# Kernel optimization log

Measured on AMD Instinct MI355X. Metric: run time of the kernel, lower is better.

Reference implementation:

```python
import jax, jax.numpy as jnp
import numpy as np

N, E, DIN, DOUT = 40000, 640000, 128, 256
BN_EPS = 1e-5  # torch BatchNorm1d default eps


def setup_inputs() -> dict:
    key = jax.random.key(0)
    ks = jax.random.split(key, 16)
    x = jax.random.normal(ks[0], (N, DIN), jnp.float32)
    edge_index = jax.random.randint(ks[1], (2, E), 0, N, dtype=jnp.int32)
    s1 = 1.0 / np.sqrt(DIN)
    s2 = 1.0 / np.sqrt(DOUT)
    return {
        "x": x,
        "edge_index": edge_index,
        "eps": jnp.zeros((), jnp.float32),  # GINConv train_eps init = 0
        "W1": jax.random.normal(ks[2], (DIN, DOUT), jnp.float32) * s1,
        "b1": jnp.zeros((DOUT,), jnp.float32),
        "g1": jnp.ones((DOUT,), jnp.float32),
        "bt1": jnp.zeros((DOUT,), jnp.float32),
        "m1": jax.random.normal(ks[3], (DOUT,), jnp.float32) * 0.1,
        "v1": jax.random.uniform(ks[4], (DOUT,), jnp.float32, 0.5, 1.5),
        "W2": jax.random.normal(ks[5], (DOUT, DOUT), jnp.float32) * s2,
        "b2": jnp.zeros((DOUT,), jnp.float32),
        "g2": jnp.ones((DOUT,), jnp.float32),
        "bt2": jnp.zeros((DOUT,), jnp.float32),
        "m2": jax.random.normal(ks[6], (DOUT,), jnp.float32) * 0.1,
        "v2": jax.random.uniform(ks[7], (DOUT,), jnp.float32, 0.5, 1.5),
        "Wres": jax.random.normal(ks[8], (DIN, DOUT), jnp.float32) * s1,
    }


def _bn(h, g, b, m, v):
    # inference-mode BatchNorm1d with running stats
    return (h - m) * jax.lax.rsqrt(v + BN_EPS) * g + b


def reference(x, edge_index, eps, W1, b1, g1, bt1, m1, v1,
              W2, b2, g2, bt2, m2, v2, Wres):
    src, dst = edge_index[0], edge_index[1]
    # GIN sum aggregation: messages x[src] scatter-added at dst
    agg = jax.ops.segment_sum(x[src], dst, num_segments=N)  # [N, DIN]
    h = (1.0 + eps) * x + agg
    h = jax.nn.relu(_bn(h @ W1 + b1, g1, bt1, m1, v1))       # [N, DOUT]
    h = jax.nn.relu(_bn(h @ W2 + b2, g2, bt2, m2, v2))       # [N, DOUT]
    # dropout is identity in eval mode; residual projection since DIN != DOUT
    return jax.nn.relu(h + x @ Wres)
```

## Files before the change

kernel.cpp:

```cpp
#include <hip/hip_runtime.h>

#define NN 40000
#define NPAD 40064
#define EE 640000
#define KDIN 128
#define KDOUT 256

#define NB 157
#define CAP 6144
#define CAPH 4096

typedef __attribute__((ext_vector_type(8))) short bf16x8;
typedef __attribute__((ext_vector_type(4))) float f32x4;

static __device__ __forceinline__ unsigned short f2bf(float f) {
    union { float f; unsigned int u; } v; v.f = f;
    unsigned int r = (v.u + 0x7FFFu + ((v.u >> 16) & 1u)) >> 16;
    return (unsigned short)r;
}
static __device__ __forceinline__ float bf2f(unsigned short h) {
    union { unsigned int u; float f; } v; v.u = ((unsigned int)h) << 16;
    return v.f;
}

#define PREP_GRID 3021
__global__ __launch_bounds__(256) void k_prep(
    const float* __restrict__ x,
    const float* __restrict__ W1, const float* __restrict__ W2,
    const float* __restrict__ Wres,
    ushort* __restrict__ xb, ushort* __restrict__ wt_all,
    int* __restrict__ cur, ushort* __restrict__ hb) {
    int b = blockIdx.x, tid = threadIdx.x;
    if (b < 2504) {
        int i = b * 256 + tid;
        int row = i >> 4;
        uint4 o = {0, 0, 0, 0};
        if (row < NN) {
            const float4* xp = (const float4*)x + (size_t)i * 2;
            float4 a = xp[0], c = xp[1];
            o.x = (unsigned)f2bf(a.x) | ((unsigned)f2bf(a.y) << 16);
            o.y = (unsigned)f2bf(a.z) | ((unsigned)f2bf(a.w) << 16);
            o.z = (unsigned)f2bf(c.x) | ((unsigned)f2bf(c.y) << 16);
            o.w = (unsigned)f2bf(c.z) | ((unsigned)f2bf(c.w) << 16);
        }
        if (row < NPAD) *(uint4*)(xb + (size_t)i * 8) = o;
    } else if (b < 3016) {
        int j = (b - 2504) * 256 + tid;
        if (j < 32768) {
            int c = j >> 7, r = j & 127;
            wt_all[j] = f2bf(W1[r * KDOUT + c]);
        } else if (j < 98304) {
            int j2 = j - 32768;
            int c = j2 >> 8, r = j2 & 255;
            wt_all[j] = f2bf(W2[r * KDOUT + c]);
        } else {
            int j3 = j - 98304;
            int c = j3 >> 7, r = j3 & 127;
            wt_all[j] = f2bf(Wres[r * KDOUT + c]);
        }
    } else if (b < 3020) {
        int idx = (b - 3016) * 256 + tid;
        ((uint4*)(hb + (size_t)NN * KDIN))[idx] = (uint4){0, 0, 0, 0};
    } else {
        if (tid < NB) cur[tid] = 0;
    }
}

__global__ __launch_bounds__(256) void k_binA(const int* __restrict__ ei,
                                              int* __restrict__ cur,
                                              unsigned int* __restrict__ recs) {
    __shared__ int cnt[160], lstart[160], lcur[160], gbase[160];
    __shared__ int sw[256];
    __shared__ unsigned int lrec[4096];
    __shared__ int laddr[4096];
    int tid = threadIdx.x;
    int e0 = blockIdx.x * 4096;
    int e1 = min(e0 + 4096, EE);
    int ns = e1 - e0;

    if (tid < NB) cnt[tid] = 0;
    __syncthreads();
    for (int s = tid; s < ns; s += 256)
        atomicAdd(&cnt[ei[EE + e0 + s] >> 8], 1);
    __syncthreads();
    sw[tid] = (tid < NB) ? cnt[tid] : 0;
    __syncthreads();
    for (int off = 1; off < 256; off <<= 1) {
        int add = (tid >= off) ? sw[tid - off] : 0;
        __syncthreads();
        sw[tid] += add;
        __syncthreads();
    }
    if (tid < NB) {
        int st = sw[tid] - cnt[tid];
        lstart[tid] = st;
        lcur[tid] = st;
        gbase[tid] = atomicAdd(&cur[tid], cnt[tid]);
    }
    __syncthreads();
    for (int s = tid; s < ns; s += 256) {
        int e = e0 + s;
        int src = ei[e];
        int dst = ei[EE + e];
        int b = dst >> 8;
        int p = atomicAdd(&lcur[b], 1);
        lrec[p] = ((unsigned int)(dst & 255) << 16) | (unsigned int)src;
        laddr[p] = b * CAP + gbase[b] + (p - lstart[b]);
    }
    __syncthreads();
    for (int s = tid; s < ns; s += 256)
        recs[laddr[s]] = lrec[s];
}

__global__ __launch_bounds__(256) void k_aggB(const unsigned int* __restrict__ recs,
                                              const int* __restrict__ cur,
                                              const ushort* __restrict__ xb,
                                              const float* __restrict__ eps,
                                              ushort* __restrict__ hb) {
    __shared__ ushort lsrc[CAPH];
    __shared__ int lcnt[128], lst[128], lcur[128];
    __shared__ int sw[256];
    int tid = threadIdx.x;
    int bi = blockIdx.x;
    int b = bi >> 3, nh = (bi >> 2) & 1, q = bi & 3;
    int cnt = cur[b];
    const unsigned int* rb = recs + (size_t)b * CAP;

    if (tid < 128) lcnt[tid] = 0;
    __syncthreads();
    for (int s = tid; s < cnt; s += 256) {
        int d = rb[s] >> 16;
        if ((d >> 7) == nh) atomicAdd(&lcnt[d & 127], 1);
    }
    __syncthreads();
    sw[tid] = (tid < 128) ? lcnt[tid] : 0;
    __syncthreads();
    for (int off = 1; off < 128; off <<= 1) {
        int add = (tid >= off) ? sw[tid - off] : 0;
        __syncthreads();
        sw[tid] += add;
        __syncthreads();
    }
    if (tid < 128) {
        int e = sw[tid] - lcnt[tid];
        lst[tid] = e;
        lcur[tid] = e;
    }
    __syncthreads();
    for (int s = tid; s < cnt; s += 256) {
        unsigned int r = rb[s];
        int d = r >> 16;
        if ((d >> 7) == nh) {
            int p = atomicAdd(&lcur[d & 127], 1);
            lsrc[p] = (ushort)(r & 0xffff);
        }
    }
    __syncthreads();

    int g = tid >> 2, lane = tid & 3;
    float s1 = 1.0f + eps[0];
    for (int d = g; d < 128; d += 64) {
        int node = b * 256 + nh * 128 + d;
        if (node >= NN) continue;
        int st = lst[d], en = st + lcnt[d];
        uint4 me = *((const uint4*)(xb + (size_t)node * KDIN) + q * 4 + lane);
        float a[8], a2[8];
        a[0] = bf2f((ushort)(me.x & 0xffff)) * s1; a[1] = bf2f((ushort)(me.x >> 16)) * s1;
        a[2] = bf2f((ushort)(me.y & 0xffff)) * s1; a[3] = bf2f((ushort)(me.y >> 16)) * s1;
        a[4] = bf2f((ushort)(me.z & 0xffff)) * s1; a[5] = bf2f((ushort)(me.z >> 16)) * s1;
        a[6] = bf2f((ushort)(me.w & 0xffff)) * s1; a[7] = bf2f((ushort)(me.w >> 16)) * s1;
#pragma unroll
        for (int i = 0; i < 8; ++i) a2[i] = 0.f;
        int e = st;
        for (; e + 1 < en; e += 2) {
            int s0 = lsrc[e], sB = lsrc[e + 1];
            uint4 v0 = *((const uint4*)(xb + (size_t)s0 * KDIN) + q * 4 + lane);
            uint4 v1 = *((const uint4*)(xb + (size_t)sB * KDIN) + q * 4 + lane);
            a[0] += bf2f((ushort)(v0.x & 0xffff)); a[1] += bf2f((ushort)(v0.x >> 16));
            a[2] += bf2f((ushort)(v0.y & 0xffff)); a[3] += bf2f((ushort)(v0.y >> 16));
            a[4] += bf2f((ushort)(v0.z & 0xffff)); a[5] += bf2f((ushort)(v0.z >> 16));
            a[6] += bf2f((ushort)(v0.w & 0xffff)); a[7] += bf2f((ushort)(v0.w >> 16));
            a2[0] += bf2f((ushort)(v1.x & 0xffff)); a2[1] += bf2f((ushort)(v1.x >> 16));
            a2[2] += bf2f((ushort)(v1.y & 0xffff)); a2[3] += bf2f((ushort)(v1.y >> 16));
            a2[4] += bf2f((ushort)(v1.z & 0xffff)); a2[5] += bf2f((ushort)(v1.z >> 16));
            a2[6] += bf2f((ushort)(v1.w & 0xffff)); a2[7] += bf2f((ushort)(v1.w >> 16));
        }
        if (e < en) {
            int s0 = lsrc[e];
            uint4 v0 = *((const uint4*)(xb + (size_t)s0 * KDIN) + q * 4 + lane);
            a[0] += bf2f((ushort)(v0.x & 0xffff)); a[1] += bf2f((ushort)(v0.x >> 16));
            a[2] += bf2f((ushort)(v0.y & 0xffff)); a[3] += bf2f((ushort)(v0.y >> 16));
            a[4] += bf2f((ushort)(v0.z & 0xffff)); a[5] += bf2f((ushort)(v0.z >> 16));
            a[6] += bf2f((ushort)(v0.w & 0xffff)); a[7] += bf2f((ushort)(v0.w >> 16));
        }
#pragma unroll
        for (int i = 0; i < 8; ++i) a[i] += a2[i];
        uint4 o;
        o.x = (unsigned)f2bf(a[0]) | ((unsigned)f2bf(a[1]) << 16);
        o.y = (unsigned)f2bf(a[2]) | ((unsigned)f2bf(a[3]) << 16);
        o.z = (unsigned)f2bf(a[4]) | ((unsigned)f2bf(a[5]) << 16);
        o.w = (unsigned)f2bf(a[6]) | ((unsigned)f2bf(a[7]) << 16);
        *((uint4*)(hb + (size_t)node * KDIN) + q * 4 + lane) = o;
    }
}


#define STAGE_WT(Wt_, Kc_, K2_)                                                 \
    for (int id = tid; id < BNT * (K2_) / 16; id += 256) {                      \
        int c = id / ((K2_) / 16);                                              \
        int koff = (id % ((K2_) / 16)) * 16;                                    \
        uint4 v = *(const uint4*)((const char*)((Wt_) + (size_t)(ncol0 + c) * (Kc_)) + koff); \
        *(uint4*)((char*)s + c * (K2_) + (koff ^ ((c & 7) << 4))) = v;          \
    }

#define MM_LOOP(A_, Kc_, K2_, acc0_, acc1_)                                     \
    {                                                                           \
        const char* a0p = (const char*)((A_) + (size_t)r0 * (Kc_)) + lq * 16;   \
        const char* a1p = a0p + 16 * (Kc_) * 2;                                 \
        for (int k0 = 0; k0 < (Kc_); k0 += 32) {                                \
            bf16x8 a0 = *(const bf16x8*)(a0p + k0 * 2);                         \
            bf16x8 a1 = *(const bf16x8*)(a1p + k0 * 2);                         \
            int kb = (k0 + lq * 8) * 2;                                         \
            _Pragma("unroll")                                                   \
            for (int nt = 0; nt < 8; ++nt) {                                    \
                int c = nt * 16 + l15;                                          \
                bf16x8 b = *(const bf16x8*)((const char*)s + c * (K2_) + (kb ^ ((c & 7) << 4))); \
                acc0_[nt] = __builtin_amdgcn_mfma_f32_16x16x32_bf16(a0, b, acc0_[nt], 0, 0, 0); \
                acc1_[nt] = __builtin_amdgcn_mfma_f32_16x16x32_bf16(a1, b, acc1_[nt], 0, 0, 0); \
            }                                                                   \
        }                                                                       \
    }

#define BNT 128

__global__ __launch_bounds__(256) void k_mm1(
    const ushort* __restrict__ A, const ushort* __restrict__ Wt,
    const float* __restrict__ bb, const float* __restrict__ g,
    const float* __restrict__ bt, const float* __restrict__ m,
    const float* __restrict__ vv, ushort* __restrict__ C) {
    __shared__ ushort s[BNT * 128];
    int tid = threadIdx.x;
    int bm = blockIdx.x >> 1, bn = blockIdx.x & 1;
    int ncol0 = bn * BNT;
    STAGE_WT(Wt, 128, 256);
    __syncthreads();
    int wid = tid >> 6, lane = tid & 63;
    int l15 = lane & 15, lq = lane >> 4;
    int r0 = bm * 128 + wid * 32 + l15;
    f32x4 acc0[8] = {}, acc1[8] = {};
    MM_LOOP(A, 128, 256, acc0, acc1);
#pragma unroll
    for (int nt = 0; nt < 8; ++nt) {
        int col = ncol0 + nt * 16 + l15;
        float sc = g[col] * rsqrtf(vv[col] + 1e-5f);
        float bo = (bb[col] - m[col]) * sc + bt[col];
        int rb = bm * 128 + wid * 32 + lq * 4;
#pragma unroll
        for (int r = 0; r < 4; ++r) {
            C[(size_t)(rb + r) * KDOUT + col] = f2bf(fmaxf(acc0[nt][r] * sc + bo, 0.f));
            C[(size_t)(rb + 16 + r) * KDOUT + col] = f2bf(fmaxf(acc1[nt][r] * sc + bo, 0.f));
        }
    }
}

__global__ __launch_bounds__(256) void k_mm2(
    const ushort* __restrict__ H1, const ushort* __restrict__ W2t,
    const ushort* __restrict__ X, const ushort* __restrict__ Wrt,
    const float* __restrict__ bb, const float* __restrict__ g,
    const float* __restrict__ bt, const float* __restrict__ m,
    const float* __restrict__ vv, float* __restrict__ OUT) {
    __shared__ ushort s[BNT * 256];
    int tid = threadIdx.x;
    int bm = blockIdx.x >> 1, bn = blockIdx.x & 1;
    int ncol0 = bn * BNT;
    int wid = tid >> 6, lane = tid & 63;
    int l15 = lane & 15, lq = lane >> 4;
    int r0 = bm * 128 + wid * 32 + l15;

    STAGE_WT(W2t, 256, 512);
    __syncthreads();
    f32x4 acc0[8] = {}, acc1[8] = {};
    MM_LOOP(H1, 256, 512, acc0, acc1);

    __syncthreads();
    STAGE_WT(Wrt, 128, 256);
    __syncthreads();
    f32x4 acd0[8] = {}, acd1[8] = {};
    MM_LOOP(X, 128, 256, acd0, acd1);

#pragma unroll
    for (int nt = 0; nt < 8; ++nt) {
        int col = ncol0 + nt * 16 + l15;
        float sc = g[col] * rsqrtf(vv[col] + 1e-5f);
        float bo = (bb[col] - m[col]) * sc + bt[col];
        int rb = bm * 128 + wid * 32 + lq * 4;
#pragma unroll
        for (int r = 0; r < 4; ++r) {
            int row0 = rb + r, row1 = rb + 16 + r;
            float t0 = fmaxf(acc0[nt][r] * sc + bo, 0.f);
            float t1 = fmaxf(acc1[nt][r] * sc + bo, 0.f);
            if (row0 < NN) OUT[(size_t)row0 * KDOUT + col] = fmaxf(t0 + acd0[nt][r], 0.f);
            if (row1 < NN) OUT[(size_t)row1 * KDOUT + col] = fmaxf(t1 + acd1[nt][r], 0.f);
        }
    }
}

extern "C" void kernel_launch(void* const* d_in, const int* in_sizes, int n_in,
                              void* d_out, int out_size, void* d_ws, size_t ws_size,
                              hipStream_t stream) {
    const float* x    = (const float*)d_in[0];
    const int*   ei   = (const int*)d_in[1];
    const float* eps  = (const float*)d_in[2];
    const float* W1   = (const float*)d_in[3];
    const float* b1   = (const float*)d_in[4];
    const float* g1   = (const float*)d_in[5];
    const float* bt1  = (const float*)d_in[6];
    const float* m1   = (const float*)d_in[7];
    const float* v1   = (const float*)d_in[8];
    const float* W2   = (const float*)d_in[9];
    const float* b2   = (const float*)d_in[10];
    const float* g2   = (const float*)d_in[11];
    const float* bt2  = (const float*)d_in[12];
    const float* m2   = (const float*)d_in[13];
    const float* v2   = (const float*)d_in[14];
    const float* Wres = (const float*)d_in[15];
    float* out = (float*)d_out;

    char* w = (char*)d_ws;
    ushort* xb  = (ushort*)w;                 w += (size_t)NPAD * KDIN * 2;
    ushort* hb  = (ushort*)w;                 w += (size_t)NPAD * KDIN * 2;
    ushort* h1b = (ushort*)w;                 w += (size_t)NPAD * KDOUT * 2;
    ushort* w1t = (ushort*)w;                 w += 256 * 128 * 2;
    ushort* w2t = (ushort*)w;                 w += 256 * 256 * 2;
    ushort* wrt = (ushort*)w;                 w += 256 * 128 * 2;
    int* cur    = (int*)w;                    w += 256 * 4;
    unsigned int* recs = (unsigned int*)w;    w += (size_t)NB * CAP * 4;

    k_prep<<<PREP_GRID, 256, 0, stream>>>(x, W1, W2, Wres, xb, w1t, cur, hb);
    k_binA<<<NB, 256, 0, stream>>>(ei, cur, recs);
    k_aggB<<<NB * 8, 256, 0, stream>>>(recs, cur, xb, eps, hb);

    const int grid = (NPAD / 128) * 2;
    k_mm1<<<grid, 256, 0, stream>>>(hb, w1t, b1, g1, bt1, m1, v1, h1b);
    k_mm2<<<grid, 256, 0, stream>>>(h1b, w2t, xb, wrt, b2, g2, bt2, m2, v2, out);
}
```

Before: 104.6 us.

## Fuse edge binning into prep kernel and gather per-chunk bins in aggregation

```diff
diff --git a/kernel.cpp b/kernel.cpp
--- a/kernel.cpp
+++ b/kernel.cpp
@@ -6,9 +6,9 @@
 #define KDIN 128
 #define KDOUT 256
 
-#define NB 157
-#define CAP 6144
-#define CAPH 4096
+#define NBIN 157
+#define BCAP 5120
+#define CAPQ 1536
 
 typedef __attribute__((ext_vector_type(8))) short bf16x8;
 typedef __attribute__((ext_vector_type(4))) float f32x4;
@@ -23,16 +23,58 @@
     return v.f;
 }
 
-#define PREP_GRID 3021
-__global__ __launch_bounds__(256) void k_prep(
+#define FRONT_GRID 3177
+__global__ __launch_bounds__(256) void k_front(
     const float* __restrict__ x,
     const float* __restrict__ W1, const float* __restrict__ W2,
-    const float* __restrict__ Wres,
+    const float* __restrict__ Wres, const int* __restrict__ ei,
     ushort* __restrict__ xb, ushort* __restrict__ wt_all,
-    int* __restrict__ cur, ushort* __restrict__ hb) {
+    unsigned int* __restrict__ recs, int* __restrict__ lmat,
+    ushort* __restrict__ hb) {
+    __shared__ unsigned int SM[4096 + 480 + 256];
     int b = blockIdx.x, tid = threadIdx.x;
-    if (b < 2504) {
-        int i = b * 256 + tid;
+    if (b < NBIN) {
+        unsigned int* lrec = SM;
+        int* cnt    = (int*)(SM + 4096);
+        int* lstart = cnt + 160;
+        int* lcur   = lstart + 160;
+        int* sw     = lcur + 160;
+        int e0 = b * 4096;
+        int ns = min(e0 + 4096, EE) - e0;
+
+        if (tid < NBIN) cnt[tid] = 0;
+        __syncthreads();
+        for (int s = tid; s < ns; s += 256)
+            atomicAdd(&cnt[ei[EE + e0 + s] >> 8], 1);
+        __syncthreads();
+        sw[tid] = (tid < NBIN) ? cnt[tid] : 0;
+        __syncthreads();
+        for (int off = 1; off < 256; off <<= 1) {
+            int add = (tid >= off) ? sw[tid - off] : 0;
+            __syncthreads();
+            sw[tid] += add;
+            __syncthreads();
+        }
+        if (tid < NBIN) {
+            int st = sw[tid] - cnt[tid];
+            lstart[tid] = st;
+            lcur[tid] = st;
+        }
+        __syncthreads();
+        for (int s = tid; s < ns; s += 256) {
+            int e = e0 + s;
+            int src = ei[e];
+            int dst = ei[EE + e];
+            int p = atomicAdd(&lcur[dst >> 8], 1);
+            lrec[p] = ((unsigned int)(dst & 255) << 16) | (unsigned int)src;
+        }
+        __syncthreads();
+        for (int s = tid; s < ns; s += 256)
+            recs[b * 4096 + s] = lrec[s];
+        if (tid < NBIN + 1)
+            lmat[b * 158 + tid] = (tid < NBIN) ? lstart[tid] : ns;
+    } else if (b < 2661) {
+        int i = (b - NBIN) * 256 + tid;
         int row = i >> 4;
         uint4 o = {0, 0, 0, 0};
         if (row < NN) {
@@ -44,8 +86,8 @@
             o.w = (unsigned)f2bf(c.z) | ((unsigned)f2bf(c.w) << 16);
         }
         if (row < NPAD) *(uint4*)(xb + (size_t)i * 8) = o;
-    } else if (b < 3016) {
-        int j = (b - 2504) * 256 + tid;
+    } else if (b < 3173) {
+        int j = (b - 2661) * 256 + tid;
         if (j < 32768) {
             int c = j >> 7, r = j & 127;
             wt_all[j] = f2bf(W1[r * KDOUT + c]);
@@ -58,150 +100,117 @@
             int c = j3 >> 7, r = j3 & 127;
             wt_all[j] = f2bf(Wres[r * KDOUT + c]);
         }
-    } else if (b < 3020) {
-        int idx = (b - 3016) * 256 + tid;
+    } else {
+        int idx = (b - 3173) * 256 + tid;
         ((uint4*)(hb + (size_t)NN * KDIN))[idx] = (uint4){0, 0, 0, 0};
-    } else {
-        if (tid < NB) cur[tid] = 0;
-    }
-}
-
-__global__ __launch_bounds__(256) void k_binA(const int* __restrict__ ei,
-                                              int* __restrict__ cur,
-                                              unsigned int* __restrict__ recs) {
-    __shared__ int cnt[160], lstart[160], lcur[160], gbase[160];
-    __shared__ int sw[256];
-    __shared__ unsigned int lrec[4096];
-    __shared__ int laddr[4096];
-    int tid = threadIdx.x;
-    int e0 = blockIdx.x * 4096;
-    int e1 = min(e0 + 4096, EE);
-    int ns = e1 - e0;
-
-    if (tid < NB) cnt[tid] = 0;
-    __syncthreads();
-    for (int s = tid; s < ns; s += 256)
-        atomicAdd(&cnt[ei[EE + e0 + s] >> 8], 1);
-    __syncthreads();
-    sw[tid] = (tid < NB) ? cnt[tid] : 0;
-    __syncthreads();
-    for (int off = 1; off < 256; off <<= 1) {
-        int add = (tid >= off) ? sw[tid - off] : 0;
-        __syncthreads();
-        sw[tid] += add;
-        __syncthreads();
-    }
-    if (tid < NB) {
-        int st = sw[tid] - cnt[tid];
-        lstart[tid] = st;
-        lcur[tid] = st;
-        gbase[tid] = atomicAdd(&cur[tid], cnt[tid]);
-    }
-    __syncthreads();
-    for (int s = tid; s < ns; s += 256) {
-        int e = e0 + s;
-        int src = ei[e];
-        int dst = ei[EE + e];
-        int b = dst >> 8;
-        int p = atomicAdd(&lcur[b], 1);
-        lrec[p] = ((unsigned int)(dst & 255) << 16) | (unsigned int)src;
-        laddr[p] = b * CAP + gbase[b] + (p - lstart[b]);
-    }
-    __syncthreads();
-    for (int s = tid; s < ns; s += 256)
-        recs[laddr[s]] = lrec[s];
+    }
 }
 
 __global__ __launch_bounds__(256) void k_aggB(const unsigned int* __restrict__ recs,
-                                              const int* __restrict__ cur,
+                                              const int* __restrict__ lmat,
                                               const ushort* __restrict__ xb,
                                               const float* __restrict__ eps,
                                               ushort* __restrict__ hb) {
-    __shared__ ushort lsrc[CAPH];
-    __shared__ int lcnt[128], lst[128], lcur[128];
+    __shared__ unsigned int lrec[BCAP];
+    __shared__ ushort lsrc[CAPQ];
+    __shared__ int lcnt[64], lst[64], lcur[64];
     __shared__ int sw[256];
     int tid = threadIdx.x;
     int bi = blockIdx.x;
-    int b = bi >> 3, nh = (bi >> 2) & 1, q = bi & 3;
-    int cnt = cur[b];
-    const unsigned int* rb = recs + (size_t)b * CAP;
-
-    if (tid < 128) lcnt[tid] = 0;
-    __syncthreads();
-    for (int s = tid; s < cnt; s += 256) {
-        int d = rb[s] >> 16;
-        if ((d >> 7) == nh) atomicAdd(&lcnt[d & 127], 1);
-    }
-    __syncthreads();
-    sw[tid] = (tid < 128) ? lcnt[tid] : 0;
-    __syncthreads();
-    for (int off = 1; off < 128; off <<= 1) {
+    int b = bi >> 4, nq = (bi >> 2) & 3, q = bi & 3;
+
+    int len = 0, s0 = 0;
+    if (tid < NBIN) {
+        s0 = lmat[tid * 158 + b];
+        len = lmat[tid * 158 + b + 1] - s0;
+    }
+    sw[tid] = len;
+    __syncthreads();
+    for (int off = 1; off < 256; off <<= 1) {
         int add = (tid >= off) ? sw[tid - off] : 0;
         __syncthreads();
         sw[tid] += add;
         __syncthreads();
     }
-    if (tid < 128) {
+    int pofs = sw[tid] - len;
+    int ctot = sw[255];
+    for (int i = 0; i < len; ++i)
+        lrec[pofs + i] = recs[tid * 4096 + s0 + i];
+    if (tid < 64) lcnt[tid] = 0;
+    __syncthreads();
+
+    for (int s = tid; s < ctot; s += 256) {
+        int d8 = lrec[s] >> 16;
+        if ((d8 >> 6) == nq) atomicAdd(&lcnt[d8 & 63], 1);
+    }
+    __syncthreads();
+    sw[tid] = (tid < 64) ? lcnt[tid] : 0;
+    __syncthreads();
+    for (int off = 1; off < 64; off <<= 1) {
+        int add = (tid >= off) ? sw[tid - off] : 0;
+        __syncthreads();
+        sw[tid] += add;
+        __syncthreads();
+    }
+    if (tid < 64) {
         int e = sw[tid] - lcnt[tid];
         lst[tid] = e;
         lcur[tid] = e;
     }
     __syncthreads();
-    for (int s = tid; s < cnt; s += 256) {
-        unsigned int r = rb[s];
-        int d = r >> 16;
-        if ((d >> 7) == nh) {
-            int p = atomicAdd(&lcur[d & 127], 1);
+    for (int s = tid; s < ctot; s += 256) {
+        unsigned int r = lrec[s];
+        int d8 = r >> 16;
+        if ((d8 >> 6) == nq) {
+            int p = atomicAdd(&lcur[d8 & 63], 1);
             lsrc[p] = (ushort)(r & 0xffff);
         }
     }
     __syncthreads();
 
     int g = tid >> 2, lane = tid & 3;
+    int node = b * 256 + nq * 64 + g;
+    if (node >= NN) return;
     float s1 = 1.0f + eps[0];
-    for (int d = g; d < 128; d += 64) {
-        int node = b * 256 + nh * 128 + d;
-        if (node >= NN) continue;
-        int st = lst[d], en = st + lcnt[d];
-        uint4 me = *((const uint4*)(xb + (size_t)node * KDIN) + q * 4 + lane);
-        float a[8], a2[8];
-        a[0] = bf2f((ushort)(me.x & 0xffff)) * s1; a[1] = bf2f((ushort)(me.x >> 16)) * s1;
-        a[2] = bf2f((ushort)(me.y & 0xffff)) * s1; a[3] = bf2f((ushort)(me.y >> 16)) * s1;
-        a[4] = bf2f((ushort)(me.z & 0xffff)) * s1; a[5] = bf2f((ushort)(me.z >> 16)) * s1;
-        a[6] = bf2f((ushort)(me.w & 0xffff)) * s1; a[7] = bf2f((ushort)(me.w >> 16)) * s1;
-#pragma unroll
-        for (int i = 0; i < 8; ++i) a2[i] = 0.f;
-        int e = st;
-        for (; e + 1 < en; e += 2) {
-            int s0 = lsrc[e], sB = lsrc[e + 1];
-            uint4 v0 = *((const uint4*)(xb + (size_t)s0 * KDIN) + q * 4 + lane);
-            uint4 v1 = *((const uint4*)(xb + (size_t)sB * KDIN) + q * 4 + lane);
-            a[0] += bf2f((ushort)(v0.x & 0xffff)); a[1] += bf2f((ushort)(v0.x >> 16));
-            a[2] += bf2f((ushort)(v0.y & 0xffff)); a[3] += bf2f((ushort)(v0.y >> 16));
-            a[4] += bf2f((ushort)(v0.z & 0xffff)); a[5] += bf2f((ushort)(v0.z >> 16));
-            a[6] += bf2f((ushort)(v0.w & 0xffff)); a[7] += bf2f((ushort)(v0.w >> 16));
-            a2[0] += bf2f((ushort)(v1.x & 0xffff)); a2[1] += bf2f((ushort)(v1.x >> 16));
-            a2[2] += bf2f((ushort)(v1.y & 0xffff)); a2[3] += bf2f((ushort)(v1.y >> 16));
-            a2[4] += bf2f((ushort)(v1.z & 0xffff)); a2[5] += bf2f((ushort)(v1.z >> 16));
-            a2[6] += bf2f((ushort)(v1.w & 0xffff)); a2[7] += bf2f((ushort)(v1.w >> 16));
-        }
-        if (e < en) {
-            int s0 = lsrc[e];
-            uint4 v0 = *((const uint4*)(xb + (size_t)s0 * KDIN) + q * 4 + lane);
-            a[0] += bf2f((ushort)(v0.x & 0xffff)); a[1] += bf2f((ushort)(v0.x >> 16));
-            a[2] += bf2f((ushort)(v0.y & 0xffff)); a[3] += bf2f((ushort)(v0.y >> 16));
-            a[4] += bf2f((ushort)(v0.z & 0xffff)); a[5] += bf2f((ushort)(v0.z >> 16));
-            a[6] += bf2f((ushort)(v0.w & 0xffff)); a[7] += bf2f((ushort)(v0.w >> 16));
-        }
-#pragma unroll
-        for (int i = 0; i < 8; ++i) a[i] += a2[i];
-        uint4 o;
-        o.x = (unsigned)f2bf(a[0]) | ((unsigned)f2bf(a[1]) << 16);
-        o.y = (unsigned)f2bf(a[2]) | ((unsigned)f2bf(a[3]) << 16);
-        o.z = (unsigned)f2bf(a[4]) | ((unsigned)f2bf(a[5]) << 16);
-        o.w = (unsigned)f2bf(a[6]) | ((unsigned)f2bf(a[7]) << 16);
-        *((uint4*)(hb + (size_t)node * KDIN) + q * 4 + lane) = o;
-    }
+    int st = lst[g], en = st + lcnt[g];
+    uint4 me = *((const uint4*)(xb + (size_t)node * KDIN) + q * 4 + lane);
+    float a[8], a2[8];
+    a[0] = bf2f((ushort)(me.x & 0xffff)) * s1; a[1] = bf2f((ushort)(me.x >> 16)) * s1;
+    a[2] = bf2f((ushort)(me.y & 0xffff)) * s1; a[3] = bf2f((ushort)(me.y >> 16)) * s1;
+    a[4] = bf2f((ushort)(me.z & 0xffff)) * s1; a[5] = bf2f((ushort)(me.z >> 16)) * s1;
+    a[6] = bf2f((ushort)(me.w & 0xffff)) * s1; a[7] = bf2f((ushort)(me.w >> 16)) * s1;
+#pragma unroll
+    for (int i = 0; i < 8; ++i) a2[i] = 0.f;
+    int e = st;
+    for (; e + 1 < en; e += 2) {
+        int sA = lsrc[e], sB = lsrc[e + 1];
+        uint4 v0 = *((const uint4*)(xb + (size_t)sA * KDIN) + q * 4 + lane);
+        uint4 v1 = *((const uint4*)(xb + (size_t)sB * KDIN) + q * 4 + lane);
+        a[0] += bf2f((ushort)(v0.x & 0xffff)); a[1] += bf2f((ushort)(v0.x >> 16));
+        a[2] += bf2f((ushort)(v0.y & 0xffff)); a[3] += bf2f((ushort)(v0.y >> 16));
+        a[4] += bf2f((ushort)(v0.z & 0xffff)); a[5] += bf2f((ushort)(v0.z >> 16));
+        a[6] += bf2f((ushort)(v0.w & 0xffff)); a[7] += bf2f((ushort)(v0.w >> 16));
+        a2[0] += bf2f((ushort)(v1.x & 0xffff)); a2[1] += bf2f((ushort)(v1.x >> 16));
+        a2[2] += bf2f((ushort)(v1.y & 0xffff)); a2[3] += bf2f((ushort)(v1.y >> 16));
+        a2[4] += bf2f((ushort)(v1.z & 0xffff)); a2[5] += bf2f((ushort)(v1.z >> 16));
+        a2[6] += bf2f((ushort)(v1.w & 0xffff)); a2[7] += bf2f((ushort)(v1.w >> 16));
+    }
+    if (e < en) {
+        int sA = lsrc[e];
+        uint4 v0 = *((const uint4*)(xb + (size_t)sA * KDIN) + q * 4 + lane);
+        a[0] += bf2f((ushort)(v0.x & 0xffff)); a[1] += bf2f((ushort)(v0.x >> 16));
+        a[2] += bf2f((ushort)(v0.y & 0xffff)); a[3] += bf2f((ushort)(v0.y >> 16));
+        a[4] += bf2f((ushort)(v0.z & 0xffff)); a[5] += bf2f((ushort)(v0.z >> 16));
+        a[6] += bf2f((ushort)(v0.w & 0xffff)); a[7] += bf2f((ushort)(v0.w >> 16));
+    }
+#pragma unroll
+    for (int i = 0; i < 8; ++i) a[i] += a2[i];
+    uint4 o;
+    o.x = (unsigned)f2bf(a[0]) | ((unsigned)f2bf(a[1]) << 16);
+    o.y = (unsigned)f2bf(a[2]) | ((unsigned)f2bf(a[3]) << 16);
+    o.z = (unsigned)f2bf(a[4]) | ((unsigned)f2bf(a[5]) << 16);
+    o.w = (unsigned)f2bf(a[6]) | ((unsigned)f2bf(a[7]) << 16);
+    *((uint4*)(hb + (size_t)node * KDIN) + q * 4 + lane) = o;
 }
 
 
@@ -333,12 +342,12 @@
     ushort* w1t = (ushort*)w;                 w += 256 * 128 * 2;
     ushort* w2t = (ushort*)w;                 w += 256 * 256 * 2;
     ushort* wrt = (ushort*)w;                 w += 256 * 128 * 2;
-    int* cur    = (int*)w;                    w += 256 * 4;
-    unsigned int* recs = (unsigned int*)w;    w += (size_t)NB * CAP * 4;
-
-    k_prep<<<PREP_GRID, 256, 0, stream>>>(x, W1, W2, Wres, xb, w1t, cur, hb);
-    k_binA<<<NB, 256, 0, stream>>>(ei, cur, recs);
-    k_aggB<<<NB * 8, 256, 0, stream>>>(recs, cur, xb, eps, hb);
+    unsigned int* recs = (unsigned int*)w;    w += (size_t)NBIN * 4096 * 4;
+    int* lmat   = (int*)w;                    w += (size_t)NBIN * 158 * 4;
+
+    k_front<<<FRONT_GRID, 256, 0, stream>>>(x, W1, W2, Wres, ei, xb, w1t,
+                                            recs, lmat, hb);
+    k_aggB<<<NBIN * 16, 256, 0, stream>>>(recs, lmat, xb, eps, hb);
 
     const int grid = (NPAD / 128) * 2;
     k_mm1<<<grid, 256, 0, stream>>>(hb, w1t, b1, g1, bt1, m1, v1, h1b);
```

Result: slower. 110.3 us (+5.4%).
